# Performance work log

Hardware: AMD Instinct MI355X
Metric: run time of the kernel (lower is better)

## Reference

```python
import jax, jax.numpy as jnp
import numpy as np

B, H, S, D = 2, 16, 2048, 64
POLAR_SCALE = 0.125
QJL_SCALE = 0.01


def setup_inputs() -> dict:
    key = jax.random.key(0)
    ks = jax.random.split(key, 5)
    shape = (B, H, S, D)
    return {
        "q": jax.random.normal(ks[0], shape, dtype=jnp.float32),
        "k_polar": jax.random.normal(ks[1], shape, dtype=jnp.float32),
        "k_qjl": jax.random.normal(ks[2], shape, dtype=jnp.float32),
        "v_polar": jax.random.normal(ks[3], shape, dtype=jnp.float32),
        "v_qjl": jax.random.normal(ks[4], shape, dtype=jnp.float32),
    }


def reference(q, k_polar, k_qjl, v_polar, v_qjl):
    head_dim = q.shape[-1]
    sm_scale = 1.0 / np.sqrt(head_dim).astype(np.float32)
    # fused dequant of K/V from polar + qjl codes
    k = k_polar * POLAR_SCALE + k_qjl * QJL_SCALE  # [B,H,S,D]
    v = v_polar * POLAR_SCALE + v_qjl * QJL_SCALE  # [B,H,S,D]
    # non-causal attention with online-softmax-equivalent stable softmax
    scores = jnp.einsum("bhsd,bhtd->bhst", q * sm_scale, k)  # [B,H,S,S]
    p = jax.nn.softmax(scores, axis=-1)
    out = jnp.einsum("bhst,bhtd->bhsd", p, v)
    return out
```

## Files before the change

kernel.cpp:

```cpp
#include <hip/hip_runtime.h>

#define SS 2048
#define DD 64
#define NBH 32
#define KVB 64
#define BQ 128
#define NIT (SS / KVB)

typedef __attribute__((ext_vector_type(4))) float f32x4;
typedef __attribute__((ext_vector_type(4))) float float4_t;
typedef __attribute__((ext_vector_type(4))) short bf16x4;
typedef __attribute__((ext_vector_type(8))) short bf16x8;
typedef __attribute__((ext_vector_type(4))) unsigned int u32x4;

typedef const __attribute__((address_space(1))) unsigned int gu32_t;
typedef __attribute__((address_space(3))) unsigned int lu32_t;

__device__ __forceinline__ unsigned short f2bf(float f) {
  unsigned u = __builtin_bit_cast(unsigned, f);
  u += 0x7fffu + ((u >> 16) & 1u);
  return (unsigned short)(u >> 16);
}

__device__ __forceinline__ unsigned cvt_pk_bf16(float lo, float hi) {
  unsigned r;
  asm("v_cvt_pk_bf16_f32 %0, %1, %2" : "=v"(r) : "v"(lo), "v"(hi));
  return r;
}

__device__ __forceinline__ f32x4 MFMA32(bf16x8 a, bf16x8 b, f32x4 c) {
  return __builtin_amdgcn_mfma_f32_16x16x32_bf16(a, b, c, 0, 0, 0);
}

__global__ void dequant_k_kernel(const float* __restrict__ kp,
                                 const float* __restrict__ kq,
                                 unsigned short* __restrict__ Kd) {
  size_t base = ((size_t)blockIdx.x * 256 + threadIdx.x) * 16;
#pragma unroll
  for (int h = 0; h < 2; ++h) {
    size_t i = base + h * 8;
    float4_t a0 = *(const float4_t*)(kp + i);
    float4_t a1 = *(const float4_t*)(kp + i + 4);
    float4_t b0 = *(const float4_t*)(kq + i);
    float4_t b1 = *(const float4_t*)(kq + i + 4);
    bf16x8 r;
#pragma unroll
    for (int j = 0; j < 4; ++j) {
      r[j] = (short)f2bf(a0[j] * 0.125f + b0[j] * 0.01f);
      r[j + 4] = (short)f2bf(a1[j] * 0.125f + b1[j] * 0.01f);
    }
    *(bf16x8*)(Kd + i) = r;
  }
}

__global__ void dequant_vt_kernel(const float* __restrict__ vp,
                                  const float* __restrict__ vq,
                                  unsigned short* __restrict__ Vt) {
  __shared__ unsigned short lds[64 * 68];
  int bh = blockIdx.x >> 5;
  int sbase = (blockIdx.x & 31) * 64;
  int t = threadIdx.x;
#pragma unroll
  for (int p = 0; p < 4; ++p) {
    int s = p * 16 + (t >> 4);
    int d4 = (t & 15) * 4;
    size_t gi = ((size_t)bh * SS + sbase + s) * DD + d4;
    float4_t a = *(const float4_t*)(vp + gi);
    float4_t b = *(const float4_t*)(vq + gi);
    bf16x4 r;
#pragma unroll
    for (int j = 0; j < 4; ++j)
      r[j] = (short)f2bf(a[j] * 0.125f + b[j] * 0.01f);
    *(bf16x4*)&lds[s * 68 + d4] = r;
  }
  __syncthreads();
#pragma unroll
  for (int p = 0; p < 2; ++p) {
    int c = p * 256 + t;
    int d = c >> 3;
    int sc = (c & 7) * 8;
    bf16x8 r;
#pragma unroll
    for (int j = 0; j < 8; ++j)
      r[j] = (short)lds[(sc + j) * 68 + d];
    *(bf16x8*)(Vt + ((size_t)bh * DD + d) * SS + sbase + sc) = r;
  }
}

__global__ __launch_bounds__(256, 2) void attn_kernel(
    const float* __restrict__ q,
    const unsigned short* __restrict__ Kd,
    const unsigned short* __restrict__ Vt,
    float* __restrict__ out) {
  __shared__ unsigned short ldsK[2][KVB * DD];
  __shared__ unsigned short ldsV[2][DD * KVB];

  int bid = blockIdx.x;
  int vb = (bid & 7) * 64 + (bid >> 3);
  int bh = vb >> 4;
  int qbase = (vb & 15) * BQ;
  int t = threadIdx.x;
  int lane = t & 63;
  int w = t >> 6;
  int g = lane >> 4;
  int qi = lane & 15;

  const unsigned short* kg = Kd + (size_t)bh * SS * DD;
  const unsigned short* vg = Vt + (size_t)bh * DD * SS;

  const unsigned short* gsK[2];
  const unsigned short* gsV[2];
  int ldso[2];
#pragma unroll
  for (int p = 0; p < 2; ++p) {
    int cc = p * 256 + t;
    int row = cc >> 3;
    int slot = (cc & 7) ^ (row & 7);
    gsK[p] = kg + (size_t)row * DD + slot * 8;
    gsV[p] = vg + (size_t)row * SS + slot * 8;
    ldso[p] = cc * 16;
  }

  auto stage = [&](int it, int b) {
#pragma unroll
    for (int p = 0; p < 2; ++p)
      __builtin_amdgcn_global_load_lds(
          (gu32_t*)(gsK[p] + (size_t)it * (KVB * DD)),
          (lu32_t*)((char*)(&ldsK[b][0]) + ldso[p]), 16, 0, 0);
#pragma unroll
    for (int p = 0; p < 2; ++p)
      __builtin_amdgcn_global_load_lds(
          (gu32_t*)(gsV[p] + it * KVB),
          (lu32_t*)((char*)(&ldsV[b][0]) + ldso[p]), 16, 0, 0);
  };

  stage(0, 0);

  const float QSCALE = 0.125f * 1.44269504088896f;

  bf16x8 qf[2][2];
  const float* qp = q + ((size_t)bh * SS + qbase + w * 32) * DD;
#pragma unroll
  for (int qt = 0; qt < 2; ++qt)
#pragma unroll
    for (int kc = 0; kc < 2; ++kc) {
      const float* p0 = qp + (qt * 16 + qi) * DD + kc * 32 + g * 8;
      float4_t a = *(const float4_t*)(p0);
      float4_t b = *(const float4_t*)(p0 + 4);
      bf16x8 f;
#pragma unroll
      for (int j = 0; j < 4; ++j) {
        f[j] = (short)f2bf(a[j] * QSCALE);
        f[j + 4] = (short)f2bf(b[j] * QSCALE);
      }
      qf[qt][kc] = f;
    }

  f32x4 oacc[2][4];
#pragma unroll
  for (int qt = 0; qt < 2; ++qt)
#pragma unroll
    for (int dt = 0; dt < 4; ++dt) oacc[qt][dt] = f32x4{0.f, 0.f, 0.f, 0.f};
  float lsum[2] = {0.f, 0.f};

  __syncthreads();

  for (int it = 0; it < NIT; ++it) {
    int cur = it & 1;
    if (it + 1 < NIT) stage(it + 1, cur ^ 1);

    const char* bK = (const char*)&ldsK[cur][0];
    const char* bV = (const char*)&ldsV[cur][0];

    f32x4 sacc[2][4];
#pragma unroll
    for (int qt = 0; qt < 2; ++qt)
#pragma unroll
      for (int mt = 0; mt < 4; ++mt) sacc[qt][mt] = f32x4{0.f, 0.f, 0.f, 0.f};
    __builtin_amdgcn_s_setprio(1);
#pragma unroll
    for (int mt = 0; mt < 4; ++mt) {
      int row = mt * 16 + qi;
#pragma unroll
      for (int kc = 0; kc < 2; ++kc) {
        int colb = (kc * 64 + g * 16) ^ ((row & 7) << 4);
        bf16x8 kf = *(const bf16x8*)(bK + row * 128 + colb);
        sacc[0][mt] = MFMA32(kf, qf[0][kc], sacc[0][mt]);
        sacc[1][mt] = MFMA32(kf, qf[1][kc], sacc[1][mt]);
      }
    }
    __builtin_amdgcn_s_setprio(0);

    bf16x8 pf[2][2];
#pragma unroll
    for (int qt = 0; qt < 2; ++qt)
#pragma unroll
      for (int c = 0; c < 2; ++c) {
        u32x4 pk;
#pragma unroll
        for (int h = 0; h < 2; ++h) {
          const f32x4 s = sacc[qt][2 * c + h];
          float p0 = __builtin_amdgcn_exp2f(s[0]);
          float p1 = __builtin_amdgcn_exp2f(s[1]);
          float p2 = __builtin_amdgcn_exp2f(s[2]);
          float p3 = __builtin_amdgcn_exp2f(s[3]);
          lsum[qt] += (p0 + p1) + (p2 + p3);
          pk[2 * h] = cvt_pk_bf16(p0, p1);
          pk[2 * h + 1] = cvt_pk_bf16(p2, p3);
        }
        pf[qt][c] = __builtin_bit_cast(bf16x8, pk);
      }

    __builtin_amdgcn_s_setprio(1);
#pragma unroll
    for (int dt = 0; dt < 4; ++dt) {
      int row = dt * 16 + qi;
      int swz = (row & 7) << 4;
#pragma unroll
      for (int c = 0; c < 2; ++c) {
        bf16x4 v0 = *(const bf16x4*)(bV + row * 128 + ((c * 64 + g * 8) ^ swz));
        bf16x4 v1 = *(const bf16x4*)(bV + row * 128 + ((c * 64 + 32 + g * 8) ^ swz));
        bf16x8 vf;
#pragma unroll
        for (int j = 0; j < 4; ++j) { vf[j] = v0[j]; vf[j + 4] = v1[j]; }
        oacc[0][dt] = MFMA32(vf, pf[0][c], oacc[0][dt]);
        oacc[1][dt] = MFMA32(vf, pf[1][c], oacc[1][dt]);
      }
    }
    __builtin_amdgcn_s_setprio(0);
    __syncthreads();
  }

  float* op = out + ((size_t)bh * SS + qbase + w * 32) * DD;
#pragma unroll
  for (int qt = 0; qt < 2; ++qt) {
    float l = lsum[qt];
    l += __shfl_xor(l, 16);
    l += __shfl_xor(l, 32);
    float rl = 1.0f / l;
#pragma unroll
    for (int dt = 0; dt < 4; ++dt) {
      f32x4 o = oacc[qt][dt] * rl;
      *(f32x4*)(op + (qt * 16 + qi) * DD + dt * 16 + g * 4) = o;
    }
  }
}

extern "C" void kernel_launch(void* const* d_in, const int* in_sizes, int n_in,
                              void* d_out, int out_size, void* d_ws, size_t ws_size,
                              hipStream_t stream) {
  const float* q  = (const float*)d_in[0];
  const float* kp = (const float*)d_in[1];
  const float* kq = (const float*)d_in[2];
  const float* vp = (const float*)d_in[3];
  const float* vq = (const float*)d_in[4];
  float* out = (float*)d_out;

  unsigned short* Kd = (unsigned short*)d_ws;
  unsigned short* Vt = Kd + (size_t)NBH * SS * DD;

  dequant_k_kernel<<<1024, 256, 0, stream>>>(kp, kq, Kd);
  dequant_vt_kernel<<<1024, 256, 0, stream>>>(vp, vq, Vt);
  attn_kernel<<<512, 256, 0, stream>>>(q, Kd, Vt, out);
}
```

Baseline: 164.0 us.

## Triple-buffer K/V LDS staging with partial vmcnt waits instead of full syncthreads

Moves the attention kernel's K/V LDS staging from double to triple buffering, prefetching two tiles ahead. Each iteration now waits only until the older tile's async global-to-LDS loads have landed (vmcnt(4)) and uses a raw barrier, rather than a full __syncthreads that drains every outstanding load. This lets memory loads overlap more with the MFMA work. It also folds the score-accumulator zeroing into the first MFMA, and adds 16KB more LDS per block, which may reduce occupancy from the requested two blocks per CU.

Measured after the change: 163.0 us. About the same (-0.6%).

```diff
diff --git a/kernel.cpp b/kernel.cpp
--- a/kernel.cpp
+++ b/kernel.cpp
@@ -92,8 +92,8 @@
     const unsigned short* __restrict__ Kd,
     const unsigned short* __restrict__ Vt,
     float* __restrict__ out) {
-  __shared__ unsigned short ldsK[2][KVB * DD];
-  __shared__ unsigned short ldsV[2][DD * KVB];
+  __shared__ unsigned short ldsK[3][KVB * DD];
+  __shared__ unsigned short ldsV[3][KVB * DD];
 
   int bid = blockIdx.x;
   int vb = (bid & 7) * 64 + (bid >> 3);
@@ -135,6 +135,7 @@
   };
 
   stage(0, 0);
+  stage(1, 1);
 
   const float QSCALE = 0.125f * 1.44269504088896f;
 
@@ -162,32 +163,24 @@
 #pragma unroll
     for (int dt = 0; dt < 4; ++dt) oacc[qt][dt] = f32x4{0.f, 0.f, 0.f, 0.f};
   float lsum[2] = {0.f, 0.f};
-
-  __syncthreads();
-
-  for (int it = 0; it < NIT; ++it) {
-    int cur = it & 1;
-    if (it + 1 < NIT) stage(it + 1, cur ^ 1);
-
-    const char* bK = (const char*)&ldsK[cur][0];
-    const char* bV = (const char*)&ldsV[cur][0];
+  const f32x4 Z4 = {0.f, 0.f, 0.f, 0.f};
+
+  auto compute = [&](int b) {
+    const char* bK = (const char*)&ldsK[b][0];
+    const char* bV = (const char*)&ldsV[b][0];
 
     f32x4 sacc[2][4];
-#pragma unroll
-    for (int qt = 0; qt < 2; ++qt)
-#pragma unroll
-      for (int mt = 0; mt < 4; ++mt) sacc[qt][mt] = f32x4{0.f, 0.f, 0.f, 0.f};
     __builtin_amdgcn_s_setprio(1);
 #pragma unroll
     for (int mt = 0; mt < 4; ++mt) {
       int row = mt * 16 + qi;
-#pragma unroll
-      for (int kc = 0; kc < 2; ++kc) {
-        int colb = (kc * 64 + g * 16) ^ ((row & 7) << 4);
-        bf16x8 kf = *(const bf16x8*)(bK + row * 128 + colb);
-        sacc[0][mt] = MFMA32(kf, qf[0][kc], sacc[0][mt]);
-        sacc[1][mt] = MFMA32(kf, qf[1][kc], sacc[1][mt]);
-      }
+      int swz = (row & 7) << 4;
+      bf16x8 kf0 = *(const bf16x8*)(bK + row * 128 + ((g * 16) ^ swz));
+      sacc[0][mt] = MFMA32(kf0, qf[0][0], Z4);
+      sacc[1][mt] = MFMA32(kf0, qf[1][0], Z4);
+      bf16x8 kf1 = *(const bf16x8*)(bK + row * 128 + ((64 + g * 16) ^ swz));
+      sacc[0][mt] = MFMA32(kf1, qf[0][1], sacc[0][mt]);
+      sacc[1][mt] = MFMA32(kf1, qf[1][1], sacc[1][mt]);
     }
     __builtin_amdgcn_s_setprio(0);
 
@@ -228,8 +221,27 @@
       }
     }
     __builtin_amdgcn_s_setprio(0);
-    __syncthreads();
-  }
+  };
+
+  asm volatile("s_waitcnt vmcnt(4)" ::: "memory");
+  __builtin_amdgcn_s_barrier();
+  __builtin_amdgcn_sched_barrier(0);
+
+  int cur = 0, nb = 2;
+  for (int it = 0; it < NIT - 2; ++it) {
+    stage(it + 2, nb);
+    compute(cur);
+    asm volatile("s_waitcnt vmcnt(4)" ::: "memory");
+    __builtin_amdgcn_s_barrier();
+    __builtin_amdgcn_sched_barrier(0);
+    cur = (cur == 2) ? 0 : cur + 1;
+    nb = (nb == 2) ? 0 : nb + 1;
+  }
+  compute(cur);
+  asm volatile("s_waitcnt vmcnt(0)" ::: "memory");
+  __builtin_amdgcn_s_barrier();
+  __builtin_amdgcn_sched_barrier(0);
+  compute((cur == 2) ? 0 : cur + 1);
 
   float* op = out + ((size_t)bh * SS + qbase + w * 32) * DD;
 #pragma unroll
```
